# Kernel tuning notes

Hardware: AMD Instinct MI355X
Metric: run time of the kernel (lower is better)

Reference implementation:

```python
import jax, jax.numpy as jnp
import numpy as np

V = 100000
IN_DIM = 128
HID_DIM = 128
OUT_DIM = 128
E = 3200000


def setup_inputs() -> dict:
    key = jax.random.key(0)
    ks = jax.random.split(key, 10)
    x = jax.random.normal(ks[0], (V, IN_DIM), dtype=jnp.float32)
    edge_index = jax.random.randint(ks[1], (2, E), 0, V, dtype=jnp.int64)
    edge_weight = jax.random.uniform(ks[2], (E,), dtype=jnp.float32)
    # GCNConv params (PyG: linear weight + bias), LayerNorm gamma/beta
    W1 = jax.random.normal(ks[3], (IN_DIM, HID_DIM), dtype=jnp.float32) * 0.02
    b1 = jnp.zeros((HID_DIM,), dtype=jnp.float32)
    g1 = jnp.ones((HID_DIM,), dtype=jnp.float32)
    beta1 = jnp.zeros((HID_DIM,), dtype=jnp.float32)
    W2 = jax.random.normal(ks[4], (HID_DIM, OUT_DIM), dtype=jnp.float32) * 0.02
    b2 = jnp.zeros((OUT_DIM,), dtype=jnp.float32)
    return {"x": x, "edge_weight": edge_weight, "W1": W1, "b1": b1,
            "g1": g1, "beta1": beta1, "W2": W2, "b2": b2,
            "edge_index": edge_index}


def _gcn_conv(x, edge_index, edge_weight, W, b):
    # PyG GCNConv: x' = D^-1/2 (A + I) D^-1/2 (x W) + b, self-loop weight 1
    num_nodes = x.shape[0]
    xw = x @ W  # (V, F_out)
    src, dst = edge_index[0], edge_index[1]
    loop = jnp.arange(num_nodes, dtype=edge_index.dtype)
    row = jnp.concatenate([src, loop])
    col = jnp.concatenate([dst, loop])
    w = jnp.concatenate([edge_weight, jnp.ones((num_nodes,), dtype=x.dtype)])
    deg = jax.ops.segment_sum(w, col, num_segments=num_nodes)
    dinv = jnp.where(deg > 0, jax.lax.rsqrt(deg), 0.0)
    norm = dinv[row] * w * dinv[col]  # per-edge coefficient
    # gather-scale-scatter aggregation into destination nodes
    out = jax.ops.segment_sum(xw[row] * norm[:, None], col, num_segments=num_nodes)
    return out + b


def _layernorm(h, gamma, beta, eps=1e-5):
    mu = jnp.mean(h, axis=-1, keepdims=True)
    var = jnp.var(h, axis=-1, keepdims=True)
    return (h - mu) * jax.lax.rsqrt(var + eps) * gamma + beta


def reference(x, edge_weight, W1, b1, g1, beta1, W2, b2, edge_index):
    h = _gcn_conv(x, edge_index, edge_weight, W1, b1)
    h = jax.nn.relu(h)
    h = _layernorm(h, g1, beta1)
    # dropout is identity in eval mode
    out = _gcn_conv(h, edge_index, edge_weight, W2, b2)
    return out
```

## Files before the change

### kernel.cpp

```cpp
#include <hip/hip_runtime.h>
#include <hip/hip_fp16.h>
#include <stdint.h>

#define NV 100000
#define NE 3200000
#define NF 128
#define CAP 96
#define NB 782
#define NBLK 512
#define CHUNK 6250

typedef unsigned int u32;
typedef _Float16 half8 __attribute__((ext_vector_type(8)));
typedef _Float16 half4 __attribute__((ext_vector_type(4)));
typedef float f32x4 __attribute__((ext_vector_type(4)));

#define OFF_PART  0ull
#define OFF_ELL   25600000ull
#define OFF_HIST  102400000ull
#define OFF_BASE  104001536ull
#define OFF_DINV  104004672ull
#define OFF_CNT   104404672ull
#define OFF_TOT   104804736ull
#define OFF_WT1   104808448ull
#define OFF_WT2   104843264ull

__device__ inline u32 detect_is64(const void* ei, int start) {
    const u32* p = (const u32*)ei;
    u32 odd = p[2 * (start + (threadIdx.x & 63)) + 1];
    unsigned long long ball = __ballot(odd == 0u);
    return (__popcll(ball) > 32) ? 1u : 0u;
}

__device__ inline int load_dst(const void* ei, u32 is64, int e) {
    return is64 ? (int)((const long long*)ei)[NE + e] : ((const int*)ei)[NE + e];
}
__device__ inline void load_edge(const void* ei, u32 is64, int e, int& s, int& d) {
    if (is64) {
        const long long* p = (const long long*)ei;
        s = (int)p[e];
        d = (int)p[NE + e];
    } else {
        const int* p = (const int*)ei;
        s = p[e];
        d = p[NE + e];
    }
}

__global__ __launch_bounds__(256) void k_hist(const void* __restrict__ ei,
                                              u32* __restrict__ hist) {
    __shared__ u32 lh[NB];
    int tid = threadIdx.x, blk = blockIdx.x;
    for (int b = tid; b < NB; b += 256) lh[b] = 0u;
    __syncthreads();
    int start = blk * CHUNK;
    u32 is64 = detect_is64(ei, start);
    for (int i = tid; i < CHUNK; i += 256) {
        int d = load_dst(ei, is64, start + i);
        atomicAdd(&lh[d >> 7], 1u);
    }
    __syncthreads();
    for (int b = tid; b < NB; b += 256) hist[(size_t)blk * NB + b] = lh[b];
}

__global__ __launch_bounds__(256) void k_scanA(u32* __restrict__ hist,
                                               u32* __restrict__ tot) {
    __shared__ u32 s[2][NBLK];
    int bin = blockIdx.x, t = threadIdx.x;
    u32 v0 = hist[(size_t)t * NB + bin];
    u32 v1 = hist[(size_t)(t + 256) * NB + bin];
    s[0][t] = v0; s[0][t + 256] = v1;
    __syncthreads();
    int src = 0;
    for (int off = 1; off < NBLK; off <<= 1) {
        int dst = src ^ 1;
        u32 a = s[src][t];       if (t >= off) a += s[src][t - off];
        u32 b = s[src][t + 256]; if (t + 256 >= off) b += s[src][t + 256 - off];
        s[dst][t] = a; s[dst][t + 256] = b;
        __syncthreads();
        src = dst;
    }
    hist[(size_t)t * NB + bin] = s[src][t] - v0;
    hist[(size_t)(t + 256) * NB + bin] = s[src][t + 256] - v1;
    if (t == 0) tot[bin] = s[src][NBLK - 1];
}

__global__ __launch_bounds__(256) void k_scanB(const u32* __restrict__ tot,
                                               u32* __restrict__ base) {
    __shared__ u32 ls[2][256];
    int t = threadIdx.x;
    u32 a[4]; u32 sum = 0;
#pragma unroll
    for (int k = 0; k < 4; ++k) {
        int i = t * 4 + k;
        a[k] = (i < NB) ? tot[i] : 0u;
        sum += a[k];
    }
    ls[0][t] = sum;
    __syncthreads();
    int src = 0;
    for (int off = 1; off < 256; off <<= 1) {
        int dst = src ^ 1;
        u32 v = ls[src][t]; if (t >= off) v += ls[src][t - off];
        ls[dst][t] = v;
        __syncthreads();
        src = dst;
    }
    u32 run = ls[src][t] - sum;
#pragma unroll
    for (int k = 0; k < 4; ++k) {
        int i = t * 4 + k;
        if (i < NB) { base[i] = run; run += a[k]; }
    }
    if (t == 255) base[NB] = run;
}

__global__ __launch_bounds__(256) void k_part(const void* __restrict__ ei,
                                              const float* __restrict__ w,
                                              const u32* __restrict__ hist,
                                              const u32* __restrict__ base,
                                              uint2* __restrict__ part) {
    __shared__ u32 cur[NB];
    int tid = threadIdx.x, blk = blockIdx.x;
    for (int b = tid; b < NB; b += 256)
        cur[b] = base[b] + hist[(size_t)blk * NB + b];
    __syncthreads();
    int start = blk * CHUNK;
    u32 is64 = detect_is64(ei, start);
    for (int i = tid; i < CHUNK; i += 256) {
        int e = start + i, s, d;
        load_edge(ei, is64, e, s, d);
        u32 idx = atomicAdd(&cur[d >> 7], 1u);
        part[idx] = make_uint2(__float_as_uint(w[e]), (u32)s | ((u32)(d & 127) << 17));
    }
}

__global__ __launch_bounds__(256) void k_build(const uint2* __restrict__ part,
                                               const u32* __restrict__ base,
                                               uint2* __restrict__ ell,
                                               float* __restrict__ dinv,
                                               u32* __restrict__ cnt) {
    __shared__ u32 lcnt[128];
    __shared__ float lws[128];
    int bin = blockIdx.x, tid = threadIdx.x;
    if (tid < 128) { lcnt[tid] = 0u; lws[tid] = 0.f; }
    __syncthreads();
    int node0 = bin << 7;
    u32 start = base[bin], end = base[bin + 1];
    for (u32 i = start + tid; i < end; i += 256) {
        uint2 rec = part[i];
        u32 src = rec.y & 0x1FFFFu;
        u32 dlo = (rec.y >> 17) & 127u;
        u32 pos = atomicAdd(&lcnt[dlo], 1u);
        atomicAdd(&lws[dlo], __uint_as_float(rec.x));
        if (pos < CAP)
            ell[(size_t)(node0 + dlo) * CAP + pos] = make_uint2(rec.x, src);
    }
    __syncthreads();
    if (tid < 128) {
        int node = node0 + tid;
        if (node < NV) {
            dinv[node] = rsqrtf(1.0f + lws[tid]);
            cnt[node] = min(lcnt[tid], (u32)CAP);
        }
    }
}

__global__ __launch_bounds__(256) void k_wconv(const float* __restrict__ W1,
                                               const float* __restrict__ W2,
                                               _Float16* __restrict__ Wt1,
                                               _Float16* __restrict__ Wt2) {
    int i = blockIdx.x * 256 + threadIdx.x;
    const float* W = (i < 128 * 128) ? W1 : W2;
    _Float16* Wt = (i < 128 * 128) ? Wt1 : Wt2;
    int j = i & (128 * 128 - 1);
    int k = j >> 7, n = j & 127;
    Wt[n * 136 + k] = (_Float16)W[k * 128 + n];
}

template <typename T>
__global__ __launch_bounds__(256) void k_gemm(const T* __restrict__ X,
                                              const _Float16* __restrict__ Wt,
                                              const float* __restrict__ dinv,
                                              __half* __restrict__ Y) {
    __shared__ _Float16 Xs[64 * 136];
    __shared__ _Float16 Ws[128 * 136];
    int tid = threadIdx.x;
    int row0 = blockIdx.x * 64;

    for (int i = tid; i < 128 * 16; i += 256) {
        int r = i >> 4, c8 = i & 15;
        *(half8*)&Ws[r * 136 + c8 * 8] = *(const half8*)&Wt[r * 136 + c8 * 8];
    }

    {
        int r = tid >> 2, q = tid & 3;
        int grow = row0 + r;
        _Float16* dst = &Xs[r * 136 + q * 32];
        if (grow < NV) {
            if constexpr (sizeof(T) == 4) {
                const float4* src = (const float4*)((const float*)X + (size_t)grow * NF + q * 32);
#pragma unroll
                for (int i = 0; i < 8; ++i) {
                    float4 v = src[i];
                    half4 hh = {(_Float16)v.x, (_Float16)v.y, (_Float16)v.z, (_Float16)v.w};
                    *(half4*)&dst[i * 4] = hh;
                }
            } else {
                const half8* src = (const half8*)((const _Float16*)X + (size_t)grow * NF + q * 32);
#pragma unroll
                for (int i = 0; i < 4; ++i) *(half8*)&dst[i * 8] = src[i];
            }
        } else {
#pragma unroll
            for (int i = 0; i < 8; ++i) *(half4*)&dst[i * 4] = (half4){0, 0, 0, 0};
        }
    }
    __syncthreads();

    int wv = tid >> 6, l = tid & 63;
    int lm = l & 15, lg = l >> 4;
    f32x4 acc[8] = {};
    const _Float16* ax = &Xs[(wv * 16 + lm) * 136 + lg * 8];
#pragma unroll
    for (int kc = 0; kc < 4; ++kc) {
        half8 a = *(const half8*)&ax[kc * 32];
#pragma unroll
        for (int n = 0; n < 8; ++n) {
            half8 b = *(const half8*)&Ws[(n * 16 + lm) * 136 + kc * 32 + lg * 8];
            acc[n] = __builtin_amdgcn_mfma_f32_16x16x32_f16(a, b, acc[n], 0, 0, 0);
        }
    }

    int rbase = row0 + wv * 16 + lg * 4;
#pragma unroll
    for (int r = 0; r < 4; ++r) {
        int row = rbase + r;
        if (row < NV) {
            float dv = dinv[row];
            __half* yr = Y + (size_t)row * NF + lm;
#pragma unroll
            for (int n = 0; n < 8; ++n)
                yr[n * 16] = __float2half(acc[n][r] * dv);
        }
    }
}

#define ACC8(g, cf)                                                         \
    {                                                                       \
        float2 f_;                                                          \
        f_ = __half22float2(*(const __half2*)&(g).x);                       \
        a0 = fmaf(cf, f_.x, a0); a1 = fmaf(cf, f_.y, a1);                   \
        f_ = __half22float2(*(const __half2*)&(g).y);                       \
        a2 = fmaf(cf, f_.x, a2); a3 = fmaf(cf, f_.y, a3);                   \
        f_ = __half22float2(*(const __half2*)&(g).z);                       \
        a4 = fmaf(cf, f_.x, a4); a5 = fmaf(cf, f_.y, a5);                   \
        f_ = __half22float2(*(const __half2*)&(g).w);                       \
        a6 = fmaf(cf, f_.x, a6); a7 = fmaf(cf, f_.y, a7);                   \
    }

template <int LN>
__global__ __launch_bounds__(256) void k_agg(const __half* __restrict__ xwh,
                                             const uint2* __restrict__ ell,
                                             const u32* __restrict__ cnt,
                                             const float* __restrict__ dinv,
                                             const float* __restrict__ bias,
                                             const float* __restrict__ gamma,
                                             const float* __restrict__ beta,
                                             void* __restrict__ outv) {
    int node = blockIdx.x * 4 + (threadIdx.x >> 6);
    int lane = threadIdx.x & 63;
    int grp = lane >> 4;
    int ch = lane & 15;
    const uint4* xw4 = (const uint4*)xwh;

    float di = dinv[node];
    uint4 sv = xw4[(size_t)node * 16 + ch];

    float a0 = 0, a1 = 0, a2 = 0, a3 = 0, a4 = 0, a5 = 0, a6 = 0, a7 = 0;

    const uint2* row = ell + (size_t)node * CAP;
    u32 c = min(cnt[node], (u32)CAP);
    for (u32 p = 0; p < c; p += 16) {
        u32 i0 = p + grp, i1 = p + 4 + grp, i2 = p + 8 + grp, i3 = p + 12 + grp;
        uint2 r0 = row[min(i0, c - 1)];
        uint2 r1 = row[min(i1, c - 1)];
        uint2 r2 = row[min(i2, c - 1)];
        uint2 r3 = row[min(i3, c - 1)];
        uint4 g0 = xw4[(size_t)(r0.y & 0x1FFFFu) * 16 + ch];
        uint4 g1 = xw4[(size_t)(r1.y & 0x1FFFFu) * 16 + ch];
        uint4 g2 = xw4[(size_t)(r2.y & 0x1FFFFu) * 16 + ch];
        uint4 g3 = xw4[(size_t)(r3.y & 0x1FFFFu) * 16 + ch];
        float c0 = (i0 < c) ? __uint_as_float(r0.x) : 0.f;
        float c1 = (i1 < c) ? __uint_as_float(r1.x) : 0.f;
        float c2 = (i2 < c) ? __uint_as_float(r2.x) : 0.f;
        float c3 = (i3 < c) ? __uint_as_float(r3.x) : 0.f;
        ACC8(g0, c0);
        ACC8(g1, c1);
        ACC8(g2, c2);
        ACC8(g3, c3);
    }

#define RED(a) a += __shfl_xor(a, 16); a += __shfl_xor(a, 32);
    RED(a0) RED(a1) RED(a2) RED(a3) RED(a4) RED(a5) RED(a6) RED(a7)
#undef RED

    {
        float2 f_;
        f_ = __half22float2(*(const __half2*)&sv.x); a0 += f_.x; a1 += f_.y;
        f_ = __half22float2(*(const __half2*)&sv.y); a2 += f_.x; a3 += f_.y;
        f_ = __half22float2(*(const __half2*)&sv.z); a4 += f_.x; a5 += f_.y;
        f_ = __half22float2(*(const __half2*)&sv.w); a6 += f_.x; a7 += f_.y;
    }

    float4 b0 = *(const float4*)&bias[ch * 8];
    float4 b1 = *(const float4*)&bias[ch * 8 + 4];
    a0 = fmaf(a0, di, b0.x); a1 = fmaf(a1, di, b0.y);
    a2 = fmaf(a2, di, b0.z); a3 = fmaf(a3, di, b0.w);
    a4 = fmaf(a4, di, b1.x); a5 = fmaf(a5, di, b1.y);
    a6 = fmaf(a6, di, b1.z); a7 = fmaf(a7, di, b1.w);

    if (LN) {
        a0 = fmaxf(a0, 0.f); a1 = fmaxf(a1, 0.f); a2 = fmaxf(a2, 0.f);
        a3 = fmaxf(a3, 0.f); a4 = fmaxf(a4, 0.f); a5 = fmaxf(a5, 0.f);
        a6 = fmaxf(a6, 0.f); a7 = fmaxf(a7, 0.f);
        float s1 = a0 + a1 + a2 + a3 + a4 + a5 + a6 + a7;
        float s2 = a0 * a0 + a1 * a1 + a2 * a2 + a3 * a3 +
                   a4 * a4 + a5 * a5 + a6 * a6 + a7 * a7;
#pragma unroll
        for (int o = 8; o > 0; o >>= 1) {
            s1 += __shfl_xor(s1, o);
            s2 += __shfl_xor(s2, o);
        }
        float mu = s1 * (1.f / 128.f);
        float var = fmaf(-mu, mu, s2 * (1.f / 128.f));
        float rstd = rsqrtf(var + 1e-5f);
        float4 gm0 = *(const float4*)&gamma[ch * 8];
        float4 gm1 = *(const float4*)&gamma[ch * 8 + 4];
        float4 bt0 = *(const float4*)&beta[ch * 8];
        float4 bt1 = *(const float4*)&beta[ch * 8 + 4];
        a0 = fmaf((a0 - mu) * rstd, gm0.x, bt0.x);
        a1 = fmaf((a1 - mu) * rstd, gm0.y, bt0.y);
        a2 = fmaf((a2 - mu) * rstd, gm0.z, bt0.z);
        a3 = fmaf((a3 - mu) * rstd, gm0.w, bt0.w);
        a4 = fmaf((a4 - mu) * rstd, gm1.x, bt1.x);
        a5 = fmaf((a5 - mu) * rstd, gm1.y, bt1.y);
        a6 = fmaf((a6 - mu) * rstd, gm1.z, bt1.z);
        a7 = fmaf((a7 - mu) * rstd, gm1.w, bt1.w);
    }

    if (grp == 0) {
        if (LN) {
            __half2 h0 = __floats2half2_rn(a0, a1);
            __half2 h1 = __floats2half2_rn(a2, a3);
            __half2 h2 = __floats2half2_rn(a4, a5);
            __half2 h3 = __floats2half2_rn(a6, a7);
            uint4 pk;
            pk.x = *(u32*)&h0; pk.y = *(u32*)&h1; pk.z = *(u32*)&h2; pk.w = *(u32*)&h3;
            *(uint4*)((__half*)outv + (size_t)node * NF + ch * 8) = pk;
        } else {
            float* o = (float*)outv + (size_t)node * NF + ch * 8;
            *(float4*)o = make_float4(a0, a1, a2, a3);
            *(float4*)(o + 4) = make_float4(a4, a5, a6, a7);
        }
    }
}

extern "C" void kernel_launch(void* const* d_in, const int* in_sizes, int n_in,
                              void* d_out, int out_size, void* d_ws, size_t ws_size,
                              hipStream_t stream) {
    const float* x  = (const float*)d_in[0];
    const float* ew = (const float*)d_in[1];
    const float* W1 = (const float*)d_in[2];
    const float* b1 = (const float*)d_in[3];
    const float* g1 = (const float*)d_in[4];
    const float* be1 = (const float*)d_in[5];
    const float* W2 = (const float*)d_in[6];
    const float* b2 = (const float*)d_in[7];
    const void*  ei = d_in[8];

    char* ws = (char*)d_ws;
    uint2*  part = (uint2*)(ws + OFF_PART);
    uint2*  ell  = (uint2*)(ws + OFF_ELL);
    u32*    hist = (u32*)(ws + OFF_HIST);
    u32*    base = (u32*)(ws + OFF_BASE);
    float*  dinv = (float*)(ws + OFF_DINV);
    u32*    cnt  = (u32*)(ws + OFF_CNT);
    u32*    tot  = (u32*)(ws + OFF_TOT);
    _Float16* wt1 = (_Float16*)(ws + OFF_WT1);
    _Float16* wt2 = (_Float16*)(ws + OFF_WT2);
    __half* xwh  = (__half*)(ws + OFF_PART);
    float*  out  = (float*)d_out;
    _Float16* h  = (_Float16*)d_out;

    const int gN4 = NV / 4;
    const int gG  = (NV + 63) / 64;

    k_hist<<<NBLK, 256, 0, stream>>>(ei, hist);
    k_scanA<<<NB, 256, 0, stream>>>(hist, tot);
    k_scanB<<<1, 256, 0, stream>>>(tot, base);
    k_part<<<NBLK, 256, 0, stream>>>(ei, ew, hist, base, part);
    k_build<<<NB, 256, 0, stream>>>(part, base, ell, dinv, cnt);
    k_wconv<<<128, 256, 0, stream>>>(W1, W2, wt1, wt2);

    k_gemm<float><<<gG, 256, 0, stream>>>(x, wt1, dinv, xwh);
    k_agg<1><<<gN4, 256, 0, stream>>>(xwh, ell, cnt, dinv, b1, g1, be1, h);
    k_gemm<_Float16><<<gG, 256, 0, stream>>>(h, wt2, dinv, xwh);
    k_agg<0><<<gN4, 256, 0, stream>>>(xwh, ell, cnt, dinv, b2, nullptr, nullptr, out);
}
```

Before: 357.0 us.

## Split second-layer features into two 64-column halves aggregated separately

The second GEMM now writes its fp16 output as two separate 64-column arrays, and the final aggregation runs as two kernels, one per half, each gathering 128-byte rows. The aim is a smaller gather working set per pass (6.4 MB instead of 12.8 MB), so more of it stays in cache during the random neighbour gathers. The cost is reading the edge list twice, an extra launch, and scattered 2-byte stores in the GEMM epilogue.

```diff
diff --git a/kernel.cpp b/kernel.cpp
--- a/kernel.cpp
+++ b/kernel.cpp
@@ -16,6 +16,7 @@
 typedef float f32x4 __attribute__((ext_vector_type(4)));
 
 #define OFF_PART  0ull
+#define OFF_XHI   12800000ull
 #define OFF_ELL   25600000ull
 #define OFF_HIST  102400000ull
 #define OFF_BASE  104001536ull
@@ -178,11 +179,12 @@
     Wt[n * 136 + k] = (_Float16)W[k * 128 + n];
 }
 
-template <typename T>
+template <typename T, int SPLIT>
 __global__ __launch_bounds__(256) void k_gemm(const T* __restrict__ X,
                                               const _Float16* __restrict__ Wt,
                                               const float* __restrict__ dinv,
-                                              __half* __restrict__ Y) {
+                                              __half* __restrict__ Ylo,
+                                              __half* __restrict__ Yhi) {
     __shared__ _Float16 Xs[64 * 136];
     __shared__ _Float16 Ws[128 * 136];
     int tid = threadIdx.x;
@@ -238,10 +240,16 @@
         int row = rbase + r;
         if (row < NV) {
             float dv = dinv[row];
-            __half* yr = Y + (size_t)row * NF + lm;
-#pragma unroll
-            for (int n = 0; n < 8; ++n)
-                yr[n * 16] = __float2half(acc[n][r] * dv);
+#pragma unroll
+            for (int n = 0; n < 8; ++n) {
+                int col = n * 16 + lm;
+                __half* yr;
+                if (SPLIT)
+                    yr = (col < 64 ? Ylo : Yhi) + (size_t)row * 64 + (col & 63);
+                else
+                    yr = Ylo + (size_t)row * NF + col;
+                *yr = __float2half(acc[n][r] * dv);
+            }
         }
     }
 }
@@ -259,15 +267,14 @@
         a6 = fmaf(cf, f_.x, a6); a7 = fmaf(cf, f_.y, a7);                   \
     }
 
-template <int LN>
-__global__ __launch_bounds__(256) void k_agg(const __half* __restrict__ xwh,
-                                             const uint2* __restrict__ ell,
-                                             const u32* __restrict__ cnt,
-                                             const float* __restrict__ dinv,
-                                             const float* __restrict__ bias,
-                                             const float* __restrict__ gamma,
-                                             const float* __restrict__ beta,
-                                             void* __restrict__ outv) {
+__global__ __launch_bounds__(256) void k_agg_ln(const __half* __restrict__ xwh,
+                                                const uint2* __restrict__ ell,
+                                                const u32* __restrict__ cnt,
+                                                const float* __restrict__ dinv,
+                                                const float* __restrict__ bias,
+                                                const float* __restrict__ gamma,
+                                                const float* __restrict__ beta,
+                                                __half* __restrict__ outh) {
     int node = blockIdx.x * 4 + (threadIdx.x >> 6);
     int lane = threadIdx.x & 63;
     int grp = lane >> 4;
@@ -320,49 +327,107 @@
     a4 = fmaf(a4, di, b1.x); a5 = fmaf(a5, di, b1.y);
     a6 = fmaf(a6, di, b1.z); a7 = fmaf(a7, di, b1.w);
 
-    if (LN) {
-        a0 = fmaxf(a0, 0.f); a1 = fmaxf(a1, 0.f); a2 = fmaxf(a2, 0.f);
-        a3 = fmaxf(a3, 0.f); a4 = fmaxf(a4, 0.f); a5 = fmaxf(a5, 0.f);
-        a6 = fmaxf(a6, 0.f); a7 = fmaxf(a7, 0.f);
-        float s1 = a0 + a1 + a2 + a3 + a4 + a5 + a6 + a7;
-        float s2 = a0 * a0 + a1 * a1 + a2 * a2 + a3 * a3 +
-                   a4 * a4 + a5 * a5 + a6 * a6 + a7 * a7;
-#pragma unroll
-        for (int o = 8; o > 0; o >>= 1) {
-            s1 += __shfl_xor(s1, o);
-            s2 += __shfl_xor(s2, o);
-        }
-        float mu = s1 * (1.f / 128.f);
-        float var = fmaf(-mu, mu, s2 * (1.f / 128.f));
-        float rstd = rsqrtf(var + 1e-5f);
-        float4 gm0 = *(const float4*)&gamma[ch * 8];
-        float4 gm1 = *(const float4*)&gamma[ch * 8 + 4];
-        float4 bt0 = *(const float4*)&beta[ch * 8];
-        float4 bt1 = *(const float4*)&beta[ch * 8 + 4];
-        a0 = fmaf((a0 - mu) * rstd, gm0.x, bt0.x);
-        a1 = fmaf((a1 - mu) * rstd, gm0.y, bt0.y);
-        a2 = fmaf((a2 - mu) * rstd, gm0.z, bt0.z);
-        a3 = fmaf((a3 - mu) * rstd, gm0.w, bt0.w);
-        a4 = fmaf((a4 - mu) * rstd, gm1.x, bt1.x);
-        a5 = fmaf((a5 - mu) * rstd, gm1.y, bt1.y);
-        a6 = fmaf((a6 - mu) * rstd, gm1.z, bt1.z);
-        a7 = fmaf((a7 - mu) * rstd, gm1.w, bt1.w);
-    }
+    a0 = fmaxf(a0, 0.f); a1 = fmaxf(a1, 0.f); a2 = fmaxf(a2, 0.f);
+    a3 = fmaxf(a3, 0.f); a4 = fmaxf(a4, 0.f); a5 = fmaxf(a5, 0.f);
+    a6 = fmaxf(a6, 0.f); a7 = fmaxf(a7, 0.f);
+    float s1 = a0 + a1 + a2 + a3 + a4 + a5 + a6 + a7;
+    float s2 = a0 * a0 + a1 * a1 + a2 * a2 + a3 * a3 +
+               a4 * a4 + a5 * a5 + a6 * a6 + a7 * a7;
+#pragma unroll
+    for (int o = 8; o > 0; o >>= 1) {
+        s1 += __shfl_xor(s1, o);
+        s2 += __shfl_xor(s2, o);
+    }
+    float mu = s1 * (1.f / 128.f);
+    float var = fmaf(-mu, mu, s2 * (1.f / 128.f));
+    float rstd = rsqrtf(var + 1e-5f);
+    float4 gm0 = *(const float4*)&gamma[ch * 8];
+    float4 gm1 = *(const float4*)&gamma[ch * 8 + 4];
+    float4 bt0 = *(const float4*)&beta[ch * 8];
+    float4 bt1 = *(const float4*)&beta[ch * 8 + 4];
+    a0 = fmaf((a0 - mu) * rstd, gm0.x, bt0.x);
+    a1 = fmaf((a1 - mu) * rstd, gm0.y, bt0.y);
+    a2 = fmaf((a2 - mu) * rstd, gm0.z, bt0.z);
+    a3 = fmaf((a3 - mu) * rstd, gm0.w, bt0.w);
+    a4 = fmaf((a4 - mu) * rstd, gm1.x, bt1.x);
+    a5 = fmaf((a5 - mu) * rstd, gm1.y, bt1.y);
+    a6 = fmaf((a6 - mu) * rstd, gm1.z, bt1.z);
+    a7 = fmaf((a7 - mu) * rstd, gm1.w, bt1.w);
 
     if (grp == 0) {
-        if (LN) {
-            __half2 h0 = __floats2half2_rn(a0, a1);
-            __half2 h1 = __floats2half2_rn(a2, a3);
-            __half2 h2 = __floats2half2_rn(a4, a5);
-            __half2 h3 = __floats2half2_rn(a6, a7);
-            uint4 pk;
-            pk.x = *(u32*)&h0; pk.y = *(u32*)&h1; pk.z = *(u32*)&h2; pk.w = *(u32*)&h3;
-            *(uint4*)((__half*)outv + (size_t)node * NF + ch * 8) = pk;
-        } else {
-            float* o = (float*)outv + (size_t)node * NF + ch * 8;
-            *(float4*)o = make_float4(a0, a1, a2, a3);
-            *(float4*)(o + 4) = make_float4(a4, a5, a6, a7);
-        }
+        __half2 h0 = __floats2half2_rn(a0, a1);
+        __half2 h1 = __floats2half2_rn(a2, a3);
+        __half2 h2 = __floats2half2_rn(a4, a5);
+        __half2 h3 = __floats2half2_rn(a6, a7);
+        uint4 pk;
+        pk.x = *(u32*)&h0; pk.y = *(u32*)&h1; pk.z = *(u32*)&h2; pk.w = *(u32*)&h3;
+        *(uint4*)(outh + (size_t)node * NF + ch * 8) = pk;
+    }
+}
+
+template <int HALF>
+__global__ __launch_bounds__(256) void k_agg_half(const __half* __restrict__ xwh,
+                                                  const uint2* __restrict__ ell,
+                                                  const u32* __restrict__ cnt,
+                                                  const float* __restrict__ dinv,
+                                                  const float* __restrict__ bias,
+                                                  float* __restrict__ out) {
+    int node = blockIdx.x * 4 + (threadIdx.x >> 6);
+    int lane = threadIdx.x & 63;
+    int rep = lane >> 3;
+    int ch = lane & 7;
+    const uint4* xw4 = (const uint4*)xwh;
+
+    float di = dinv[node];
+    uint4 sv = xw4[(size_t)node * 8 + ch];
+
+    float a0 = 0, a1 = 0, a2 = 0, a3 = 0, a4 = 0, a5 = 0, a6 = 0, a7 = 0;
+
+    const uint2* row = ell + (size_t)node * CAP;
+    u32 c = min(cnt[node], (u32)CAP);
+    for (u32 p = 0; p < c; p += 32) {
+        u32 i0 = p + rep, i1 = p + 8 + rep, i2 = p + 16 + rep, i3 = p + 24 + rep;
+        uint2 r0 = row[min(i0, c - 1)];
+        uint2 r1 = row[min(i1, c - 1)];
+        uint2 r2 = row[min(i2, c - 1)];
+        uint2 r3 = row[min(i3, c - 1)];
+        uint4 g0 = xw4[(size_t)(r0.y & 0x1FFFFu) * 8 + ch];
+        uint4 g1 = xw4[(size_t)(r1.y & 0x1FFFFu) * 8 + ch];
+        uint4 g2 = xw4[(size_t)(r2.y & 0x1FFFFu) * 8 + ch];
+        uint4 g3 = xw4[(size_t)(r3.y & 0x1FFFFu) * 8 + ch];
+        float c0 = (i0 < c) ? __uint_as_float(r0.x) : 0.f;
+        float c1 = (i1 < c) ? __uint_as_float(r1.x) : 0.f;
+        float c2 = (i2 < c) ? __uint_as_float(r2.x) : 0.f;
+        float c3 = (i3 < c) ? __uint_as_float(r3.x) : 0.f;
+        ACC8(g0, c0);
+        ACC8(g1, c1);
+        ACC8(g2, c2);
+        ACC8(g3, c3);
+    }
+
+#define RED(a) a += __shfl_xor(a, 8); a += __shfl_xor(a, 16); a += __shfl_xor(a, 32);
+    RED(a0) RED(a1) RED(a2) RED(a3) RED(a4) RED(a5) RED(a6) RED(a7)
+#undef RED
+
+    {
+        float2 f_;
+        f_ = __half22float2(*(const __half2*)&sv.x); a0 += f_.x; a1 += f_.y;
+        f_ = __half22float2(*(const __half2*)&sv.y); a2 += f_.x; a3 += f_.y;
+        f_ = __half22float2(*(const __half2*)&sv.z); a4 += f_.x; a5 += f_.y;
+        f_ = __half22float2(*(const __half2*)&sv.w); a6 += f_.x; a7 += f_.y;
+    }
+
+    float4 b0 = *(const float4*)&bias[HALF * 64 + ch * 8];
+    float4 b1 = *(const float4*)&bias[HALF * 64 + ch * 8 + 4];
+    a0 = fmaf(a0, di, b0.x); a1 = fmaf(a1, di, b0.y);
+    a2 = fmaf(a2, di, b0.z); a3 = fmaf(a3, di, b0.w);
+    a4 = fmaf(a4, di, b1.x); a5 = fmaf(a5, di, b1.y);
+    a6 = fmaf(a6, di, b1.z); a7 = fmaf(a7, di, b1.w);
+
+    if (rep == 0) {
+        float* o = out + (size_t)node * NF + HALF * 64 + ch * 8;
+        *(float4*)o = make_float4(a0, a1, a2, a3);
+        *(float4*)(o + 4) = make_float4(a4, a5, a6, a7);
     }
 }
 
@@ -390,6 +455,8 @@
     _Float16* wt1 = (_Float16*)(ws + OFF_WT1);
     _Float16* wt2 = (_Float16*)(ws + OFF_WT2);
     __half* xwh  = (__half*)(ws + OFF_PART);
+    __half* xlo  = (__half*)(ws + OFF_PART);
+    __half* xhi  = (__half*)(ws + OFF_XHI);
     float*  out  = (float*)d_out;
     _Float16* h  = (_Float16*)d_out;
 
@@ -403,8 +470,9 @@
     k_build<<<NB, 256, 0, stream>>>(part, base, ell, dinv, cnt);
     k_wconv<<<128, 256, 0, stream>>>(W1, W2, wt1, wt2);
 
-    k_gemm<float><<<gG, 256, 0, stream>>>(x, wt1, dinv, xwh);
-    k_agg<1><<<gN4, 256, 0, stream>>>(xwh, ell, cnt, dinv, b1, g1, be1, h);
-    k_gemm<_Float16><<<gG, 256, 0, stream>>>(h, wt2, dinv, xwh);
-    k_agg<0><<<gN4, 256, 0, stream>>>(xwh, ell, cnt, dinv, b2, nullptr, nullptr, out);
-}
+    k_gemm<float, 0><<<gG, 256, 0, stream>>>(x, wt1, dinv, (__half*)xwh, nullptr);
+    k_agg_ln<<<gN4, 256, 0, stream>>>(xwh, ell, cnt, dinv, b1, g1, be1, (__half*)h);
+    k_gemm<_Float16, 1><<<gG, 256, 0, stream>>>(h, wt2, dinv, xlo, xhi);
+    k_agg_half<0><<<gN4, 256, 0, stream>>>(xlo, ell, cnt, dinv, b2, out);
+    k_agg_half<1><<<gN4, 256, 0, stream>>>(xhi, ell, cnt, dinv, b2, out);
+}
```

Measured after the change: 353.4 us. About the same (-1.0%).
